# Optimization experiments

Hardware: AMD Instinct MI355X
Metric: run time of the kernel (lower is better)

## Reference

```python
import jax, jax.numpy as jnp
import numpy as np

EMB = 1024
FF = 4096
NE = 8
TOPK = 2
TEMP = 1.0


def setup_inputs() -> dict:
    key = jax.random.key(0)
    ks = jax.random.split(key, 8)
    s_emb = 1.0 / np.sqrt(EMB)
    s_ff = 1.0 / np.sqrt(FF)
    x = jax.random.normal(ks[0], (4, 2048, EMB), dtype=jnp.float32)
    gate_W = jax.random.uniform(ks[1], (EMB, NE), minval=-s_emb, maxval=s_emb, dtype=jnp.float32)
    gate_b = jax.random.uniform(ks[2], (NE,), minval=-s_emb, maxval=s_emb, dtype=jnp.float32)
    W1 = jax.random.uniform(ks[3], (NE, EMB, FF), minval=-s_emb, maxval=s_emb, dtype=jnp.float32)
    b1 = jax.random.uniform(ks[4], (NE, FF), minval=-s_emb, maxval=s_emb, dtype=jnp.float32)
    W2 = jax.random.uniform(ks[5], (NE, FF, EMB), minval=-s_ff, maxval=s_ff, dtype=jnp.float32)
    b2 = jax.random.uniform(ks[6], (NE, EMB), minval=-s_ff, maxval=s_ff, dtype=jnp.float32)
    return {"x": x, "gate_W": gate_W, "gate_b": gate_b, "W1": W1, "b1": b1, "W2": W2, "b2": b2}


def reference(x, gate_W, gate_b, W1, b1, W2, b2):
    B, S, D = x.shape
    xf = x.reshape(-1, D)  # [T, D]
    T = xf.shape[0]

    gate_logits = (xf @ gate_W + gate_b) / TEMP            # [T, E]
    gate_scores = jax.nn.softmax(gate_logits, axis=-1)     # [T, E]
    topk_scores, topk_idx = jax.lax.top_k(gate_scores, TOPK)
    topk_scores = topk_scores / jnp.sum(topk_scores, axis=-1, keepdims=True)

    # combine_weights[t, e] = sum_i topk_scores[t, i] * (topk_idx[t, i] == e)
    onehot = jax.nn.one_hot(topk_idx, NE, dtype=xf.dtype)  # [T, K, E]
    combine = jnp.einsum('tk,tke->te', topk_scores, onehot)  # [T, E]

    # Dense per-expert FFN (dropout is identity in eval): h = gelu(x W1 + b1); y = h W2 + b2
    h = jax.nn.gelu(jnp.einsum('td,edf->etf', xf, W1) + b1[:, None, :], approximate=False)
    y = jnp.einsum('etf,efd->etd', h, W2) + b2[:, None, :]  # [E, T, D]
    out = jnp.einsum('te,etd->td', combine, y).reshape(B, S, D)

    # Load-balance auxiliary loss
    expert_counts = jnp.sum(onehot, axis=(0, 1))            # [E]
    expert_fraction = expert_counts / (T * TOPK)
    routing_weights = jnp.mean(gate_scores, axis=0)
    aux_loss = NE * jnp.sum(expert_fraction * routing_weights)
    return out, aux_loss
```

## Files before the change

kernel.cpp:

```cpp
#include <hip/hip_runtime.h>
#include <math.h>

#define EMB 1024
#define FF  4096
#define NE  8
#define TTOK 8192

typedef __attribute__((ext_vector_type(4))) float  f32x4;
typedef __attribute__((ext_vector_type(8))) __bf16 bf16x8;
typedef __attribute__((ext_vector_type(4))) __bf16 bf16x4;

#define MAXROWS  18432

#define WS_COUNTS  0
#define WS_CURSORS 1024
#define WS_SSUM    1056
#define WS_NTILES  2080
#define WS_BASE    2084
#define WS_TILE_E  2176
#define WS_TILE_RB 2816
#define WS_TKIDX   4096
#define WS_TKW     69632
#define WS_SLOT    135168
#define WS_TOKID   200704
#define WS_ROWW    274432
#define WS_BIG2    350208

#define SZ_W1T ((size_t)NE * EMB * FF * 2)
#define SZ_W2T ((size_t)NE * EMB * FF * 2)
#define SZ_XB  ((size_t)TTOK * EMB * 2)
#define SZ_H   ((size_t)MAXROWS * FF * 2)
#define SZ_XG  ((size_t)MAXROWS * EMB * 2)
#define SZ_Y2  ((size_t)MAXROWS * EMB * 2)

__device__ inline f32x4 fzero() { f32x4 v = {0.f, 0.f, 0.f, 0.f}; return v; }

__device__ __forceinline__ void gl16(const void* g, void* l) {
    __builtin_amdgcn_global_load_lds(
        (const __attribute__((address_space(1))) void*)g,
        (__attribute__((address_space(3))) void*)l, 16, 0, 0);
}

#define DSR(dst, addr, off) \
    asm volatile("ds_read_b128 %0, %1 offset:" #off : "=v"(dst) : "v"(addr))

__device__ __forceinline__ float gelu_f(float v) {
    float u = fabsf(v) * 0.70710678118654752f;
    float p = 1.0f + u * (0.278393f + u * (0.230389f + u * (0.000972f + u * 0.078108f)));
    p = p * p; p = p * p;
    float er = 1.0f - 1.0f / p;
    float s = (v >= 0.0f) ? er : -er;
    return 0.5f * v * (1.0f + s);
}

__global__ __launch_bounds__(256) void gate_kernel(
    const float* __restrict__ x, const float* __restrict__ gW, const float* __restrict__ gb,
    int* counts, float* ssum, int* tk_idx, float* tk_w, __bf16* __restrict__ xb)
{
    int wave = threadIdx.x >> 6;
    int lane = threadIdx.x & 63;
    int t = blockIdx.x * 4 + wave;

    float acc[NE];
#pragma unroll
    for (int e = 0; e < NE; e++) acc[e] = 0.f;

    const float* xr = x + (size_t)t * EMB;
    __bf16* xbr = xb + (size_t)t * EMB;
#pragma unroll
    for (int i = 0; i < 4; i++) {
        int d0 = i * 256 + lane * 4;
        f32x4 xv = *(const f32x4*)(xr + d0);
        bf16x4 cv;
#pragma unroll
        for (int q = 0; q < 4; q++) cv[q] = (__bf16)xv[q];
        *(bf16x4*)(xbr + d0) = cv;
#pragma unroll
        for (int j = 0; j < 4; j++) {
            const float* wrow = gW + (size_t)(d0 + j) * NE;
            float xs = xv[j];
#pragma unroll
            for (int e = 0; e < NE; e++) acc[e] += xs * wrow[e];
        }
    }
#pragma unroll
    for (int e = 0; e < NE; e++) {
#pragma unroll
        for (int off = 32; off; off >>= 1) acc[e] += __shfl_xor(acc[e], off, 64);
    }
    if (lane == 0) {
        float sc[NE];
        float m = -1e30f;
        for (int e = 0; e < NE; e++) { sc[e] = acc[e] + gb[e]; m = fmaxf(m, sc[e]); }
        float sum = 0.f;
        for (int e = 0; e < NE; e++) { sc[e] = expf(sc[e] - m); sum += sc[e]; }
        float inv = 1.f / sum;
        for (int e = 0; e < NE; e++) sc[e] *= inv;
        int i0 = 0; float s0 = sc[0];
        for (int e = 1; e < NE; e++) if (sc[e] > s0) { s0 = sc[e]; i0 = e; }
        int i1 = -1; float s1 = -1e30f;
        for (int e = 0; e < NE; e++) if (e != i0 && sc[e] > s1) { s1 = sc[e]; i1 = e; }
        float rn = 1.f / (s0 + s1);
        tk_idx[2 * t]     = i0;  tk_idx[2 * t + 1] = i1;
        tk_w[2 * t]       = s0 * rn;  tk_w[2 * t + 1] = s1 * rn;
        int slot = blockIdx.x & 31;
        atomicAdd(&counts[i0 * 32 + slot], 1);
        atomicAdd(&counts[i1 * 32 + slot], 1);
        for (int e = 0; e < NE; e++) atomicAdd(&ssum[e * 32 + slot], sc[e]);
    }
}

__global__ void route_build_kernel(const int* counts, const float* ssum,
                                   int* ntiles, int* base, int* tile_e, int* tile_rb,
                                   float* out_aux)
{
    if (threadIdx.x != 0 || blockIdx.x != 0) return;
    int total = 0, tiles = 0;
    float aux = 0.f;
    for (int e = 0; e < NE; e++) {
        int c = 0; float ss = 0.f;
        for (int j = 0; j < 32; j++) { c += counts[e * 32 + j]; ss += ssum[e * 32 + j]; }
        base[e] = total;
        int nt = (c + 255) >> 8;
        for (int i = 0; i < nt; i++) { tile_e[tiles] = e; tile_rb[tiles] = total + (i << 8); tiles++; }
        total += nt << 8;
        aux += ((float)c / (float)(TTOK * 2)) * (ss / (float)TTOK);
    }
    *ntiles = tiles;
    *out_aux = aux * (float)NE;
}

__global__ __launch_bounds__(256) void scatter_kernel(
    const int* __restrict__ tk_idx, const float* __restrict__ tk_w,
    const int* __restrict__ base, int* cursors, int* token_id, float* roww,
    int* slot_of)
{
    int t = blockIdx.x * 256 + threadIdx.x;
#pragma unroll
    for (int k = 0; k < 2; k++) {
        int e = tk_idx[2 * t + k];
        int pos = atomicAdd(&cursors[e], 1);
        int slot = base[e] + pos;
        token_id[slot] = t;
        roww[slot] = tk_w[2 * t + k];
        slot_of[2 * t + k] = slot;
    }
}

__global__ __launch_bounds__(256) void pack_x_kernel(
    const __bf16* __restrict__ xb, const int* __restrict__ token_id,
    __bf16* __restrict__ xg)
{
    int tid = threadIdx.x;
    int slot = blockIdx.x * 2 + (tid >> 7);
    int off = (tid & 127) * 8;
    int tok = token_id[slot];
    uint4 v = {0u, 0u, 0u, 0u};
    if (tok >= 0) v = *(const uint4*)(xb + (size_t)tok * EMB + off);
    *(uint4*)(xg + (size_t)slot * EMB + off) = v;
}

__global__ __launch_bounds__(256) void combine_kernel(
    const __bf16* __restrict__ y0, const __bf16* __restrict__ y1, int nsplit,
    const int* __restrict__ slot_of,
    const int* __restrict__ tk_idx, const float* __restrict__ tk_w,
    const float* __restrict__ b2, float* __restrict__ out)
{
    int t = blockIdx.x;
    int dq = threadIdx.x * 4;
    int s0 = slot_of[2 * t], s1 = slot_of[2 * t + 1];
    int e0 = tk_idx[2 * t], e1 = tk_idx[2 * t + 1];
    float w0 = tk_w[2 * t], w1 = tk_w[2 * t + 1];
    bf16x4 va = *(const bf16x4*)(y0 + (size_t)s0 * EMB + dq);
    bf16x4 vb = *(const bf16x4*)(y0 + (size_t)s1 * EMB + dq);
    f32x4 ya, yb;
#pragma unroll
    for (int q = 0; q < 4; q++) { ya[q] = (float)va[q]; yb[q] = (float)vb[q]; }
    if (nsplit == 2) {
        bf16x4 za = *(const bf16x4*)(y1 + (size_t)s0 * EMB + dq);
        bf16x4 zb = *(const bf16x4*)(y1 + (size_t)s1 * EMB + dq);
#pragma unroll
        for (int q = 0; q < 4; q++) { ya[q] += (float)za[q]; yb[q] += (float)zb[q]; }
    }
    f32x4 ba = *(const f32x4*)(b2 + (size_t)e0 * EMB + dq);
    f32x4 bb = *(const f32x4*)(b2 + (size_t)e1 * EMB + dq);
    f32x4 r;
#pragma unroll
    for (int q = 0; q < 4; q++) r[q] = w0 * (ya[q] + ba[q]) + w1 * (yb[q] + bb[q]);
    *(f32x4*)(out + (size_t)t * EMB + dq) = r;
}

__global__ __launch_bounds__(256) void transpose_cvt2_kernel(
    const float* __restrict__ W1, __bf16* __restrict__ W1T,
    const float* __restrict__ W2, __bf16* __restrict__ W2T)
{
    int f = blockIdx.x;
    int which = f >> 13; f &= 8191;
    int e = f >> 10; f &= 1023;
    int R, C, bx, by;
    const float* src; __bf16* dst;
    if (which == 0) { R = EMB; C = FF;  bx = f & 15; by = f >> 4; src = W1; dst = W1T; }
    else            { R = FF;  C = EMB; bx = f & 63; by = f >> 6; src = W2; dst = W2T; }
    src += (size_t)e * R * C;
    dst += (size_t)e * R * C;
    __shared__ __bf16 Ls[64 * 72];
    int t = threadIdx.x;
    int r0 = bx * 64, c0 = by * 64;
    int ri = t >> 4, cj = (t & 15) * 4;
#pragma unroll
    for (int p = 0; p < 4; p++) {
        int r = ri + p * 16;
        f32x4 v = *(const f32x4*)(src + (size_t)(r0 + r) * C + c0 + cj);
#pragma unroll
        for (int q = 0; q < 4; q++) Ls[(cj + q) * 72 + r] = (__bf16)v[q];
    }
    __syncthreads();
    int c = t >> 2, rq = (t & 3) * 16;
    bf16x8 a = *(bf16x8*)&Ls[c * 72 + rq];
    bf16x8 b = *(bf16x8*)&Ls[c * 72 + rq + 8];
    *(bf16x8*)(dst + (size_t)(c0 + c) * R + r0 + rq) = a;
    *(bf16x8*)(dst + (size_t)(c0 + c) * R + r0 + rq + 8) = b;
}


template <bool PACKED>
__global__ __launch_bounds__(256, 3) void gemm1_8p(
    const __bf16* __restrict__ xsrc, const __bf16* __restrict__ W1T,
    const float* __restrict__ b1,
    const int* __restrict__ token_id, const int* __restrict__ tile_e,
    const int* __restrict__ tile_rb, const int* __restrict__ ntiles,
    __bf16* __restrict__ h)
{
    extern __shared__ __bf16 lds[];
    int flat = blockIdx.x;
    int c8 = flat & 7, r = flat >> 3;
    int sti = r >> 5, nb = r & 31;
    int st = c8 * 18 + sti;
    if (st >= *ntiles * 2) return;
    int e = tile_e[st >> 1];
    int rb = tile_rb[st >> 1] + (st & 1) * 128;
    int n0 = nb * 128;

    int tid = threadIdx.x, lane = tid & 63, wid = tid >> 6;
    int wr = wid >> 1, wc = wid & 1;
    int cl = lane & 15, cq = lane >> 4;

    int srow1 = ((tid >> 6) << 4) | ((tid & 63) >> 2);
    int schunk = (tid & 3) ^ ((tid >> 3) & 3);
    const __bf16* ag[2];
#pragma unroll
    for (int hm = 0; hm < 2; hm++) {
        int row = srow1 + hm * 64;
        if (PACKED) {
            ag[hm] = xsrc + (size_t)(rb + row) * EMB + schunk * 8;
        } else {
            int tok = token_id[rb + row];
            if (tok < 0) tok = 0;
            ag[hm] = xsrc + (size_t)tok * EMB + schunk * 8;
        }
    }
    const __bf16* bg[2];
#pragma unroll
    for (int hn = 0; hn < 2; hn++)
        bg[hn] = W1T + ((size_t)e * FF + (size_t)(n0 + srow1 + hn * 64)) * EMB + schunk * 8;

    int sdA0 = wid * 512, sdA1 = 2048 + wid * 512;
    int sdB0 = 4096 + wid * 512, sdB1 = 6144 + wid * 512;

    uint32_t lb = (uint32_t)(uintptr_t)(__attribute__((address_space(3))) __bf16*)lds;
    int xoffe = (cq ^ ((cl >> 1) & 3)) * 8;
    uint32_t ab0 = lb + 2u * (uint32_t)(wr * 2048 + cl * 32 + xoffe);
    uint32_t bb0 = lb + 2u * (uint32_t)(4096 + wc * 2048 + cl * 32 + xoffe);

    f32x4 acc[4][4];
#pragma unroll
    for (int i = 0; i < 4; i++)
#pragma unroll
        for (int j = 0; j < 4; j++) acc[i][j] = fzero();

    const int NT = EMB / 32;
#pragma unroll
    for (int t0 = 0; t0 < 2; t0++) {
        __bf16* bp = lds + t0 * 8192;
        int k0 = t0 * 32;
        gl16(ag[0] + k0, bp + sdA0);
        gl16(ag[1] + k0, bp + sdA1);
        gl16(bg[0] + k0, bp + sdB0);
        gl16(bg[1] + k0, bp + sdB1);
    }
    asm volatile("s_waitcnt vmcnt(4)" ::: "memory");
    __builtin_amdgcn_s_barrier();

    int cb = 0;
#pragma unroll 1
    for (int t = 0; t < NT; t++) {
        uint32_t cboff = (uint32_t)cb * 16384u;
        uint32_t aaddr = ab0 + cboff, baddr = bb0 + cboff;
        bf16x8 b[4], a[4];
        DSR(b[0], baddr, 0);    DSR(b[1], baddr, 1024);
        DSR(b[2], baddr, 2048); DSR(b[3], baddr, 3072);
        DSR(a[0], aaddr, 0);    DSR(a[1], aaddr, 1024);
        DSR(a[2], aaddr, 2048); DSR(a[3], aaddr, 3072);

        int kt = t + 2;
        if (kt < NT) {
            int sb = cb + 2; if (sb >= 3) sb -= 3;
            __bf16* sp = lds + sb * 8192;
            int ko = kt * 32;
            gl16(ag[0] + ko, sp + sdA0);
            gl16(ag[1] + ko, sp + sdA1);
            gl16(bg[0] + ko, sp + sdB0);
            gl16(bg[1] + ko, sp + sdB1);
        }

        asm volatile("s_waitcnt lgkmcnt(0)" ::: "memory");
        __builtin_amdgcn_sched_barrier(0);
        __builtin_amdgcn_s_setprio(1);
#pragma unroll
        for (int mi = 0; mi < 4; mi++)
#pragma unroll
            for (int ni = 0; ni < 4; ni++)
                acc[mi][ni] = __builtin_amdgcn_mfma_f32_16x16x32_bf16(a[mi], b[ni], acc[mi][ni], 0, 0, 0);
        __builtin_amdgcn_s_setprio(0);

        if (t < NT - 2)       { asm volatile("s_waitcnt vmcnt(4)" ::: "memory"); }
        else if (t == NT - 2) { asm volatile("s_waitcnt vmcnt(0)" ::: "memory"); }
        if (t < NT - 1) __builtin_amdgcn_s_barrier();
        cb = cb + 1; if (cb >= 3) cb = 0;
    }

    const float* b1g = b1 + (size_t)e * FF + n0;
#pragma unroll
    for (int mi = 0; mi < 4; mi++) {
#pragma unroll
        for (int ni = 0; ni < 4; ni++) {
            int col = wc * 64 + ni * 16 + cl;
            float bias = b1g[col];
#pragma unroll
            for (int j = 0; j < 4; j++) {
                int row = wr * 64 + mi * 16 + cq * 4 + j;
                float v = acc[mi][ni][j] + bias;
                h[(size_t)(rb + row) * FF + n0 + col] = (__bf16)gelu_f(v);
            }
        }
    }
}

__global__ __launch_bounds__(256, 3) void gemm2_8p(
    const __bf16* __restrict__ h, const __bf16* __restrict__ W2T,
    const int* __restrict__ tile_e, const int* __restrict__ tile_rb,
    const int* __restrict__ ntiles,
    __bf16* __restrict__ y0, __bf16* __restrict__ y1, int nsplit)
{
    extern __shared__ __bf16 lds[];
    int flat = blockIdx.x;
    int c8 = flat & 7, r = flat >> 3;
    int z = r / 144; int r144 = r - z * 144;
    int sti = r144 >> 3, nb = r144 & 7;
    int st = c8 * 18 + sti;
    if (st >= *ntiles * 2) return;
    int e = tile_e[st >> 1];
    int rb = tile_rb[st >> 1] + (st & 1) * 128;
    int n0 = nb * 128;
    int KC = FF / nsplit;
    int koff = z * KC;
    __bf16* y = z ? y1 : y0;

    int tid = threadIdx.x, lane = tid & 63, wid = tid >> 6;
    int wr = wid >> 1, wc = wid & 1;
    int cl = lane & 15, cq = lane >> 4;

    int srow1 = ((tid >> 6) << 4) | ((tid & 63) >> 2);
    int schunk = (tid & 3) ^ ((tid >> 3) & 3);
    const __bf16* ag[2];
#pragma unroll
    for (int hm = 0; hm < 2; hm++)
        ag[hm] = h + (size_t)(rb + srow1 + hm * 64) * FF + koff + schunk * 8;
    const __bf16* bg[2];
#pragma unroll
    for (int hn = 0; hn < 2; hn++)
        bg[hn] = W2T + ((size_t)e * EMB + (size_t)(n0 + srow1 + hn * 64)) * FF + koff + schunk * 8;

    int sdA0 = wid * 512, sdA1 = 2048 + wid * 512;
    int sdB0 = 4096 + wid * 512, sdB1 = 6144 + wid * 512;

    uint32_t lb = (uint32_t)(uintptr_t)(__attribute__((address_space(3))) __bf16*)lds;
    int xoffe = (cq ^ ((cl >> 1) & 3)) * 8;
    uint32_t ab0 = lb + 2u * (uint32_t)(wr * 2048 + cl * 32 + xoffe);
    uint32_t bb0 = lb + 2u * (uint32_t)(4096 + wc * 2048 + cl * 32 + xoffe);

    f32x4 acc[4][4];
#pragma unroll
    for (int i = 0; i < 4; i++)
#pragma unroll
        for (int j = 0; j < 4; j++) acc[i][j] = fzero();

    const int NT = KC / 32;
#pragma unroll
    for (int t0 = 0; t0 < 2; t0++) {
        __bf16* bp = lds + t0 * 8192;
        int k0 = t0 * 32;
        gl16(ag[0] + k0, bp + sdA0);
        gl16(ag[1] + k0, bp + sdA1);
        gl16(bg[0] + k0, bp + sdB0);
        gl16(bg[1] + k0, bp + sdB1);
    }
    asm volatile("s_waitcnt vmcnt(4)" ::: "memory");
    __builtin_amdgcn_s_barrier();

    int cb = 0;
#pragma unroll 1
    for (int t = 0; t < NT; t++) {
        uint32_t cboff = (uint32_t)cb * 16384u;
        uint32_t aaddr = ab0 + cboff, baddr = bb0 + cboff;
        bf16x8 b[4], a[4];
        DSR(b[0], baddr, 0);    DSR(b[1], baddr, 1024);
        DSR(b[2], baddr, 2048); DSR(b[3], baddr, 3072);
        DSR(a[0], aaddr, 0);    DSR(a[1], aaddr, 1024);
        DSR(a[2], aaddr, 2048); DSR(a[3], aaddr, 3072);

        int kt = t + 2;
        if (kt < NT) {
            int sb = cb + 2; if (sb >= 3) sb -= 3;
            __bf16* sp = lds + sb * 8192;
            int ko = kt * 32;
            gl16(ag[0] + ko, sp + sdA0);
            gl16(ag[1] + ko, sp + sdA1);
            gl16(bg[0] + ko, sp + sdB0);
            gl16(bg[1] + ko, sp + sdB1);
        }

        asm volatile("s_waitcnt lgkmcnt(0)" ::: "memory");
        __builtin_amdgcn_sched_barrier(0);
        __builtin_amdgcn_s_setprio(1);
#pragma unroll
        for (int mi = 0; mi < 4; mi++)
#pragma unroll
            for (int ni = 0; ni < 4; ni++)
                acc[mi][ni] = __builtin_amdgcn_mfma_f32_16x16x32_bf16(a[mi], b[ni], acc[mi][ni], 0, 0, 0);
        __builtin_amdgcn_s_setprio(0);

        if (t < NT - 2)       { asm volatile("s_waitcnt vmcnt(4)" ::: "memory"); }
        else if (t == NT - 2) { asm volatile("s_waitcnt vmcnt(0)" ::: "memory"); }
        if (t < NT - 1) __builtin_amdgcn_s_barrier();
        cb = cb + 1; if (cb >= 3) cb = 0;
    }

#pragma unroll
    for (int mi = 0; mi < 4; mi++) {
#pragma unroll
        for (int ni = 0; ni < 4; ni++) {
            int col = wc * 64 + ni * 16 + cl;
#pragma unroll
            for (int j = 0; j < 4; j++) {
                int row = wr * 64 + mi * 16 + cq * 4 + j;
                y[(size_t)(rb + row) * EMB + n0 + col] = (__bf16)acc[mi][ni][j];
            }
        }
    }
}

extern "C" void kernel_launch(void* const* d_in, const int* in_sizes, int n_in,
                              void* d_out, int out_size, void* d_ws, size_t ws_size,
                              hipStream_t stream)
{
    const float* x   = (const float*)d_in[0];
    const float* gW  = (const float*)d_in[1];
    const float* gb  = (const float*)d_in[2];
    const float* W1  = (const float*)d_in[3];
    const float* b1  = (const float*)d_in[4];
    const float* W2  = (const float*)d_in[5];
    const float* b2  = (const float*)d_in[6];
    float* out = (float*)d_out;

    char* ws = (char*)d_ws;
    int*   counts  = (int*)(ws + WS_COUNTS);
    int*   cursors = (int*)(ws + WS_CURSORS);
    float* ssum    = (float*)(ws + WS_SSUM);
    int*   ntiles  = (int*)(ws + WS_NTILES);
    int*   base    = (int*)(ws + WS_BASE);
    int*   tile_e  = (int*)(ws + WS_TILE_E);
    int*   tile_rb = (int*)(ws + WS_TILE_RB);
    int*   tk_idx  = (int*)(ws + WS_TKIDX);
    float* tk_w    = (float*)(ws + WS_TKW);
    int*   slot_of = (int*)(ws + WS_SLOT);
    int*   token_id= (int*)(ws + WS_TOKID);
    float* roww    = (float*)(ws + WS_ROWW);

    __bf16* W1T  = (__bf16*)(ws + WS_BIG2);
    __bf16* xb   = (__bf16*)(ws + WS_BIG2 + SZ_W1T);
    __bf16* W2T  = (__bf16*)(ws + WS_BIG2 + SZ_W1T + SZ_XB);
    __bf16* hbuf = (__bf16*)(ws + WS_BIG2 + SZ_W1T + SZ_XB + SZ_W2T);
    size_t fixedend = WS_BIG2 + SZ_W1T + SZ_XB + SZ_W2T;

    __bf16* y0 = (__bf16*)(ws + WS_BIG2);
    __bf16* xg = (__bf16*)(ws + fixedend + SZ_H);
    bool packed = (ws_size >= fixedend + SZ_H + SZ_XG);
    __bf16* y1 = (__bf16*)(ws + fixedend + SZ_H + (packed ? SZ_XG : 0));
    int nsplit = (ws_size >= fixedend + SZ_H + (packed ? SZ_XG : 0) + SZ_Y2) ? 2 : 1;

    hipFuncSetAttribute((const void*)gemm1_8p<true>,  hipFuncAttributeMaxDynamicSharedMemorySize, 49152);
    hipFuncSetAttribute((const void*)gemm1_8p<false>, hipFuncAttributeMaxDynamicSharedMemorySize, 49152);
    hipFuncSetAttribute((const void*)gemm2_8p, hipFuncAttributeMaxDynamicSharedMemorySize, 49152);

    hipMemsetAsync(ws + WS_COUNTS, 0, 2080, stream);
    hipMemsetAsync(ws + WS_TOKID, 0xFF, (size_t)MAXROWS * 4, stream);

    transpose_cvt2_kernel<<<16384, 256, 0, stream>>>(W1, W1T, W2, W2T);

    gate_kernel<<<TTOK / 4, 256, 0, stream>>>(x, gW, gb, counts, ssum, tk_idx, tk_w, xb);
    route_build_kernel<<<1, 64, 0, stream>>>(counts, ssum, ntiles, base, tile_e, tile_rb,
                                             out + (size_t)TTOK * EMB);
    scatter_kernel<<<TTOK / 256, 256, 0, stream>>>(tk_idx, tk_w, base, cursors, token_id, roww, slot_of);

    if (packed) {
        pack_x_kernel<<<MAXROWS / 2, 256, 0, stream>>>(xb, token_id, xg);
        gemm1_8p<true><<<8 * 18 * 32, 256, 49152, stream>>>(
            xg, W1T, b1, token_id, tile_e, tile_rb, ntiles, hbuf);
    } else {
        gemm1_8p<false><<<8 * 18 * 32, 256, 49152, stream>>>(
            xb, W1T, b1, token_id, tile_e, tile_rb, ntiles, hbuf);
    }
    gemm2_8p<<<8 * 18 * 8 * nsplit, 256, 49152, stream>>>(
        hbuf, W2T, tile_e, tile_rb, ntiles, y0, y1, nsplit);
    combine_kernel<<<TTOK, 256, 0, stream>>>(y0, y1, nsplit, slot_of, tk_idx, tk_w, b2, out);
}
```

Measured before the change: 687.4 us.

## Enlarge gemm2 tiles to 256x256 with 4-stage LDS pipeline; swizzle gemm1 blocks

The down-projection GEMM moves from 128x128 tiles with 256 threads and a 3-buffer pipeline to 256x256 tiles with 512 threads (8 waves, each computing 128x64), a 4-buffer LDS ring of 128KB and a 3-deep prefetch. The aim is to double operand reuse per loaded byte and cut global and L2 traffic. The cost is fewer blocks and only one block per CU because of the LDS footprint. Separately, gemm1's block index is remapped so groups of 8 column blocks walk across all row tiles, to improve L2 locality of the weight columns.

```diff
diff --git a/kernel.cpp b/kernel.cpp
--- a/kernel.cpp
+++ b/kernel.cpp
@@ -234,7 +234,10 @@
     extern __shared__ __bf16 lds[];
     int flat = blockIdx.x;
     int c8 = flat & 7, r = flat >> 3;
-    int sti = r >> 5, nb = r & 31;
+    int nbg = r / 144;
+    int rem = r - nbg * 144;
+    int sti = rem >> 3;
+    int nb  = (nbg << 3) | (rem & 7);
     int st = c8 * 18 + sti;
     if (st >= *ntiles * 2) return;
     int e = tile_e[st >> 1];
@@ -346,7 +349,7 @@
     }
 }
 
-__global__ __launch_bounds__(256, 3) void gemm2_8p(
+__global__ __launch_bounds__(512, 2) void gemm2_8p(
     const __bf16* __restrict__ h, const __bf16* __restrict__ W2T,
     const int* __restrict__ tile_e, const int* __restrict__ tile_rb,
     const int* __restrict__ ntiles,
@@ -355,74 +358,73 @@
     extern __shared__ __bf16 lds[];
     int flat = blockIdx.x;
     int c8 = flat & 7, r = flat >> 3;
-    int z = r / 144; int r144 = r - z * 144;
-    int sti = r144 >> 3, nb = r144 & 7;
-    int st = c8 * 18 + sti;
-    if (st >= *ntiles * 2) return;
-    int e = tile_e[st >> 1];
-    int rb = tile_rb[st >> 1] + (st & 1) * 128;
-    int n0 = nb * 128;
+    int z = r / 36; int r36 = r - z * 36;
+    int mti = r36 >> 2, nb = r36 & 3;
+    int mt = c8 * 9 + mti;
+    if (mt >= *ntiles) return;
+    int e = tile_e[mt], rb = tile_rb[mt];
+    int n0 = nb * 256;
     int KC = FF / nsplit;
     int koff = z * KC;
     __bf16* y = z ? y1 : y0;
 
     int tid = threadIdx.x, lane = tid & 63, wid = tid >> 6;
-    int wr = wid >> 1, wc = wid & 1;
+    int wr = wid >> 2, wc = wid & 3;
     int cl = lane & 15, cq = lane >> 4;
 
-    int srow1 = ((tid >> 6) << 4) | ((tid & 63) >> 2);
+    int srow = tid >> 2;
     int schunk = (tid & 3) ^ ((tid >> 3) & 3);
     const __bf16* ag[2];
 #pragma unroll
     for (int hm = 0; hm < 2; hm++)
-        ag[hm] = h + (size_t)(rb + srow1 + hm * 64) * FF + koff + schunk * 8;
+        ag[hm] = h + (size_t)(rb + hm * 128 + srow) * FF + koff + schunk * 8;
     const __bf16* bg[2];
 #pragma unroll
     for (int hn = 0; hn < 2; hn++)
-        bg[hn] = W2T + ((size_t)e * EMB + (size_t)(n0 + srow1 + hn * 64)) * FF + koff + schunk * 8;
-
-    int sdA0 = wid * 512, sdA1 = 2048 + wid * 512;
-    int sdB0 = 4096 + wid * 512, sdB1 = 6144 + wid * 512;
+        bg[hn] = W2T + ((size_t)e * EMB + (size_t)(n0 + hn * 128 + srow)) * FF + koff + schunk * 8;
+
+    int sdA0 = wid * 512, sdA1 = 4096 + wid * 512;
+    int sdB0 = 8192 + wid * 512, sdB1 = 12288 + wid * 512;
 
     uint32_t lb = (uint32_t)(uintptr_t)(__attribute__((address_space(3))) __bf16*)lds;
     int xoffe = (cq ^ ((cl >> 1) & 3)) * 8;
-    uint32_t ab0 = lb + 2u * (uint32_t)(wr * 2048 + cl * 32 + xoffe);
-    uint32_t bb0 = lb + 2u * (uint32_t)(4096 + wc * 2048 + cl * 32 + xoffe);
-
-    f32x4 acc[4][4];
-#pragma unroll
-    for (int i = 0; i < 4; i++)
+    uint32_t ab0 = lb + 2u * (uint32_t)(wr * 4096 + cl * 32 + xoffe);
+    uint32_t bb0 = lb + 2u * (uint32_t)(8192 + (wc >> 1) * 4096 + ((wc & 1) * 64 + cl) * 32 + xoffe);
+
+    f32x4 acc[8][4];
+#pragma unroll
+    for (int i = 0; i < 8; i++)
 #pragma unroll
         for (int j = 0; j < 4; j++) acc[i][j] = fzero();
 
     const int NT = KC / 32;
 #pragma unroll
-    for (int t0 = 0; t0 < 2; t0++) {
-        __bf16* bp = lds + t0 * 8192;
+    for (int t0 = 0; t0 < 3; t0++) {
+        __bf16* bp = lds + t0 * 16384;
         int k0 = t0 * 32;
         gl16(ag[0] + k0, bp + sdA0);
         gl16(ag[1] + k0, bp + sdA1);
         gl16(bg[0] + k0, bp + sdB0);
         gl16(bg[1] + k0, bp + sdB1);
     }
-    asm volatile("s_waitcnt vmcnt(4)" ::: "memory");
+    asm volatile("s_waitcnt vmcnt(8)" ::: "memory");
     __builtin_amdgcn_s_barrier();
 
-    int cb = 0;
 #pragma unroll 1
     for (int t = 0; t < NT; t++) {
-        uint32_t cboff = (uint32_t)cb * 16384u;
+        uint32_t cboff = (uint32_t)(t & 3) * 32768u;
         uint32_t aaddr = ab0 + cboff, baddr = bb0 + cboff;
-        bf16x8 b[4], a[4];
+        bf16x8 b[4], a[8];
         DSR(b[0], baddr, 0);    DSR(b[1], baddr, 1024);
         DSR(b[2], baddr, 2048); DSR(b[3], baddr, 3072);
         DSR(a[0], aaddr, 0);    DSR(a[1], aaddr, 1024);
         DSR(a[2], aaddr, 2048); DSR(a[3], aaddr, 3072);
-
-        int kt = t + 2;
+        DSR(a[4], aaddr, 4096); DSR(a[5], aaddr, 5120);
+        DSR(a[6], aaddr, 6144); DSR(a[7], aaddr, 7168);
+
+        int kt = t + 3;
         if (kt < NT) {
-            int sb = cb + 2; if (sb >= 3) sb -= 3;
-            __bf16* sp = lds + sb * 8192;
+            __bf16* sp = lds + (kt & 3) * 16384;
             int ko = kt * 32;
             gl16(ag[0] + ko, sp + sdA0);
             gl16(ag[1] + ko, sp + sdA1);
@@ -434,26 +436,26 @@
         __builtin_amdgcn_sched_barrier(0);
         __builtin_amdgcn_s_setprio(1);
 #pragma unroll
-        for (int mi = 0; mi < 4; mi++)
+        for (int mi = 0; mi < 8; mi++)
 #pragma unroll
             for (int ni = 0; ni < 4; ni++)
                 acc[mi][ni] = __builtin_amdgcn_mfma_f32_16x16x32_bf16(a[mi], b[ni], acc[mi][ni], 0, 0, 0);
         __builtin_amdgcn_s_setprio(0);
 
-        if (t < NT - 2)       { asm volatile("s_waitcnt vmcnt(4)" ::: "memory"); }
+        if (t < NT - 3)       { asm volatile("s_waitcnt vmcnt(8)" ::: "memory"); }
+        else if (t == NT - 3) { asm volatile("s_waitcnt vmcnt(4)" ::: "memory"); }
         else if (t == NT - 2) { asm volatile("s_waitcnt vmcnt(0)" ::: "memory"); }
         if (t < NT - 1) __builtin_amdgcn_s_barrier();
-        cb = cb + 1; if (cb >= 3) cb = 0;
-    }
-
-#pragma unroll
-    for (int mi = 0; mi < 4; mi++) {
+    }
+
+#pragma unroll
+    for (int mi = 0; mi < 8; mi++) {
 #pragma unroll
         for (int ni = 0; ni < 4; ni++) {
             int col = wc * 64 + ni * 16 + cl;
 #pragma unroll
             for (int j = 0; j < 4; j++) {
-                int row = wr * 64 + mi * 16 + cq * 4 + j;
+                int row = wr * 128 + mi * 16 + cq * 4 + j;
                 y[(size_t)(rb + row) * EMB + n0 + col] = (__bf16)acc[mi][ni][j];
             }
         }
@@ -501,7 +503,7 @@
 
     hipFuncSetAttribute((const void*)gemm1_8p<true>,  hipFuncAttributeMaxDynamicSharedMemorySize, 49152);
     hipFuncSetAttribute((const void*)gemm1_8p<false>, hipFuncAttributeMaxDynamicSharedMemorySize, 49152);
-    hipFuncSetAttribute((const void*)gemm2_8p, hipFuncAttributeMaxDynamicSharedMemorySize, 49152);
+    hipFuncSetAttribute((const void*)gemm2_8p, hipFuncAttributeMaxDynamicSharedMemorySize, 131072);
 
     hipMemsetAsync(ws + WS_COUNTS, 0, 2080, stream);
     hipMemsetAsync(ws + WS_TOKID, 0xFF, (size_t)MAXROWS * 4, stream);
@@ -521,7 +523,7 @@
         gemm1_8p<false><<<8 * 18 * 32, 256, 49152, stream>>>(
             xb, W1T, b1, token_id, tile_e, tile_rb, ntiles, hbuf);
     }
-    gemm2_8p<<<8 * 18 * 8 * nsplit, 256, 49152, stream>>>(
+    gemm2_8p<<<8 * 9 * 4 * nsplit, 512, 131072, stream>>>(
         hbuf, W2T, tile_e, tile_rb, ntiles, y0, y1, nsplit);
     combine_kernel<<<TTOK, 256, 0, stream>>>(y0, y1, nsplit, slot_of, tk_idx, tk_w, b2, out);
 }
```

Result: no change. 685.6 us (-0.3%).
